# Performance work log

Measured on AMD Instinct MI355X. Metric: run time of the kernel, lower is better.

The kernel has to match this reference:

```python
import jax, jax.numpy as jnp
import numpy as np

B, S, H = 4, 2048, 1024
NH = 16
DH = H // NH  # 64


def setup_inputs() -> dict:
    key = jax.random.key(0)
    ks = jax.random.split(key, 11)
    s = 1.0 / np.sqrt(H)
    inp = {
        "key": jax.random.normal(ks[0], (B, S, H), jnp.float32),
        "value": jax.random.normal(ks[1], (B, S, H), jnp.float32),
        "query": jax.random.normal(ks[2], (B, S, H), jnp.float32),
        # linear_layers[0] -> applied to query, [1] -> key, [2] -> value
        "wq": jax.random.normal(ks[3], (H, H), jnp.float32) * s,
        "bq": jnp.zeros((H,), jnp.float32),
        "wk": jax.random.normal(ks[4], (H, H), jnp.float32) * s,
        "bk": jnp.zeros((H,), jnp.float32),
        "wv": jax.random.normal(ks[5], (H, H), jnp.float32) * s,
        "bv": jnp.zeros((H,), jnp.float32),
        "wo": jax.random.normal(ks[6], (H, H), jnp.float32) * s,
        "bo": jnp.zeros((H,), jnp.float32),
    }
    return inp


def reference(key, value, query, wq, bq, wk, bk, wv, bv, wo, bo):
    # QKV projections; split heads -> [B, NH, S, DH]
    def proj(x, w, b):
        y = jnp.einsum("bsh,hd->bsd", x, w) + b
        return y.reshape(B, S, NH, DH).transpose(0, 2, 1, 3)

    q = proj(query, wq, bq)
    k = proj(key, wk, bk)
    v = proj(value, wv, bv)

    scores = jnp.einsum("bnqd,bnkd->bnqk", q, k) / jnp.sqrt(jnp.float32(DH))
    probs = jax.nn.softmax(scores, axis=-1)  # dropout p=0 -> identity
    out = jnp.einsum("bnqk,bnkd->bnqd", probs, v)
    out = out.transpose(0, 2, 1, 3).reshape(B, S, H)
    return jnp.einsum("bsh,hd->bsd", out, wo) + bo
```

## Files before the change

### kernel.cpp

```cpp
#include <hip/hip_runtime.h>
#include <hip/hip_bf16.h>

constexpr int kB = 4, kS = 2048, kH = 1024, kNH = 16, kDH = 64;
constexpr int kM = kB * kS;

typedef short short8 __attribute__((ext_vector_type(8)));
typedef float f32x4 __attribute__((ext_vector_type(4)));

__device__ inline unsigned int pack2bf16(float lo, float hi) {
  __hip_bfloat162 h;
  h.x = __float2bfloat16(lo);
  h.y = __float2bfloat16(hi);
  unsigned int u;
  __builtin_memcpy(&u, &h, 4);
  return u;
}

__device__ inline void gload_lds16(const unsigned short* g, unsigned short* l) {
  auto* gp = (const __attribute__((address_space(1))) unsigned int*)(uintptr_t)g;
  auto* lp = (__attribute__((address_space(3))) unsigned int*)(unsigned int)(uintptr_t)l;
  __builtin_amdgcn_global_load_lds(gp, lp, 16, 0, 0);
}

__global__ __launch_bounds__(256) void f32_to_bf16_vec(
    const float* __restrict__ in, __hip_bfloat16* __restrict__ out) {
  const int i = blockIdx.x * 256 + threadIdx.x;
  const float4 v = ((const float4*)in)[i];
  union { __hip_bfloat16 h[4]; uint2 u; } p;
  p.h[0] = __float2bfloat16(v.x);
  p.h[1] = __float2bfloat16(v.y);
  p.h[2] = __float2bfloat16(v.z);
  p.h[3] = __float2bfloat16(v.w);
  ((uint2*)out)[i] = p.u;
}

__global__ __launch_bounds__(256) void transpose4_f32_to_bf16(
    const float* __restrict__ w0, const float* __restrict__ w1,
    const float* __restrict__ w2, const float* __restrict__ w3,
    __hip_bfloat16* __restrict__ o0, __hip_bfloat16* __restrict__ o1,
    __hip_bfloat16* __restrict__ o2, __hip_bfloat16* __restrict__ o3) {
  const int z = blockIdx.z;
  const float* in = z == 0 ? w0 : z == 1 ? w1 : z == 2 ? w2 : w3;
  __hip_bfloat16* out = z == 0 ? o0 : z == 1 ? o1 : z == 2 ? o2 : o3;
  constexpr int R = kH, C = kH;
  __shared__ float t[32][33];
  const int r0 = blockIdx.y * 32, c0 = blockIdx.x * 32;
  const int tx = threadIdx.x, ty = threadIdx.y;
#pragma unroll
  for (int i = 0; i < 32; i += 8)
    t[ty + i][tx] = in[(size_t)(r0 + ty + i) * C + c0 + tx];
  __syncthreads();
#pragma unroll
  for (int i = 0; i < 32; i += 8)
    out[(size_t)(c0 + ty + i) * R + r0 + tx] = __float2bfloat16(t[tx][ty + i]);
}

template <int MODE, typename OutT>
__global__ __launch_bounds__(256) void gemm_mfma(
    const unsigned short* __restrict__ A,
    const unsigned short* __restrict__ Bt,
    const float* __restrict__ bias, OutT* __restrict__ C,
    int M, int N, int K, float oscale) {
  __shared__ unsigned short sA[2][128 * 32];
  __shared__ unsigned short sB[2][128 * 32];
  const int tid = threadIdx.x;
  const int wave = tid >> 6, lane = tid & 63;
  const int n16 = lane & 15, quad = lane >> 4;
  const int m0 = blockIdx.y * 128, n0 = blockIdx.x * 128;
  const int rh = (wave >> 1) * 64, ch = (wave & 1) * 64;

  const int srow = 32 * wave + (lane >> 2);
  const int sk = (lane & 3) * 8;
  const unsigned short* gA = A + (size_t)(m0 + srow) * K + sk;
  const unsigned short* gB = Bt + (size_t)(n0 + srow) * K + sk;

  const f32x4 zero4 = {0.f, 0.f, 0.f, 0.f};
  f32x4 acc[4][4];
#pragma unroll
  for (int i = 0; i < 4; ++i)
#pragma unroll
    for (int j = 0; j < 4; ++j) acc[i][j] = zero4;

#pragma unroll
  for (int j = 0; j < 2; ++j) {
    gload_lds16(gA + (size_t)(16 * j) * K, &sA[0][(32 * wave + 16 * j) * 32]);
    gload_lds16(gB + (size_t)(16 * j) * K, &sB[0][(32 * wave + 16 * j) * 32]);
  }
  __syncthreads();

  int cur = 0;
  for (int k0 = 0; k0 < K; k0 += 32) {
    const int kn = (k0 + 32 < K) ? k0 + 32 : 0;
#pragma unroll
    for (int j = 0; j < 2; ++j) {
      gload_lds16(gA + (size_t)(16 * j) * K + kn,
                  &sA[cur ^ 1][(32 * wave + 16 * j) * 32]);
      gload_lds16(gB + (size_t)(16 * j) * K + kn,
                  &sB[cur ^ 1][(32 * wave + 16 * j) * 32]);
    }

    short8 af[4], bfr[4];
#pragma unroll
    for (int i = 0; i < 4; ++i)
      af[i] = *(const short8*)&sA[cur][(rh + i * 16 + n16) * 32 + quad * 8];
#pragma unroll
    for (int i = 0; i < 4; ++i)
      bfr[i] = *(const short8*)&sB[cur][(ch + i * 16 + n16) * 32 + quad * 8];
#pragma unroll
    for (int mi = 0; mi < 4; ++mi)
#pragma unroll
      for (int ni = 0; ni < 4; ++ni)
        acc[mi][ni] = __builtin_amdgcn_mfma_f32_16x16x32_bf16(
            af[mi], bfr[ni], acc[mi][ni], 0, 0, 0);

    __syncthreads();
    cur ^= 1;
  }

#pragma unroll
  for (int ni = 0; ni < 4; ++ni) {
    const int n = n0 + ch + ni * 16 + n16;
    const float bv = bias[n];
#pragma unroll
    for (int mi = 0; mi < 4; ++mi) {
      if constexpr (MODE == 2) {
        const int m = m0 + rh + mi * 16 + quad * 4;
        const int bb = m >> 11, ss = m & 2047;
        const int hh = n >> 6, dd = n & 63;
        const size_t idx = ((size_t)(bb * kNH + hh) * kDH + dd) * kS + ss;
        uint2 w;
        w.x = pack2bf16((acc[mi][ni][0] + bv) * oscale,
                        (acc[mi][ni][1] + bv) * oscale);
        w.y = pack2bf16((acc[mi][ni][2] + bv) * oscale,
                        (acc[mi][ni][3] + bv) * oscale);
        *(uint2*)&C[idx] = w;
      } else {
#pragma unroll
        for (int r = 0; r < 4; ++r) {
          const int m = m0 + rh + mi * 16 + quad * 4 + r;
          const float v = (acc[mi][ni][r] + bv) * oscale;
          size_t idx;
          if constexpr (MODE == 1) {
            const int bb = m >> 11, ss = m & 2047;
            const int hh = n >> 6, dd = n & 63;
            idx = ((size_t)(bb * kNH + hh) * kS + ss) * kDH + dd;
          } else {
            idx = (size_t)m * N + n;
          }
          C[idx] = (OutT)v;
        }
      }
    }
  }
}

__global__ __launch_bounds__(256) void attn_mfma(
    const unsigned short* __restrict__ Q, const unsigned short* __restrict__ K,
    const unsigned short* __restrict__ V, __hip_bfloat16* __restrict__ ctx) {
  __shared__ unsigned short sK[64][72];
  __shared__ unsigned short sVT[64][72];
  __shared__ unsigned short sP[4][16][72];

  const int tid = threadIdx.x;
  const int wave = tid >> 6, lane = tid & 63;
  const int n16 = lane & 15, quad = lane >> 4;
  const int bh = blockIdx.y;
  const int q0 = blockIdx.x * 64;
  const unsigned short* Qb = Q + (size_t)bh * (kS * kDH);
  const unsigned short* Kb = K + (size_t)bh * (kS * kDH);
  const unsigned short* Vb = V + (size_t)bh * (kS * kDH);

  short8 qf[2];
  {
    const size_t qoff = (size_t)(q0 + wave * 16 + n16) * kDH + quad * 8;
    qf[0] = *(const short8*)(Qb + qoff);
    qf[1] = *(const short8*)(Qb + qoff + 32);
  }

  float l_part = 0.f;
  f32x4 oacc[4];
  const f32x4 zero4 = {0.f, 0.f, 0.f, 0.f};
#pragma unroll
  for (int d = 0; d < 4; ++d) oacc[d] = zero4;

  const int srow = tid >> 2, scol = (tid & 3) * 16;

  uint4 ka, kb, va, vb;
  auto loadtile = [&](int kk) {
    ka = *(const uint4*)(Kb + (size_t)(kk + srow) * kDH + scol);
    kb = *(const uint4*)(Kb + (size_t)(kk + srow) * kDH + scol + 8);
    va = *(const uint4*)(Vb + (size_t)srow * kS + kk + scol);
    vb = *(const uint4*)(Vb + (size_t)srow * kS + kk + scol + 8);
  };
  auto writetile = [&]() {
    *(uint4*)&sK[srow][scol] = ka;
    *(uint4*)&sK[srow][scol + 8] = kb;
    *(uint4*)&sVT[srow][scol] = va;
    *(uint4*)&sVT[srow][scol + 8] = vb;
  };

  loadtile(0);
  writetile();
  __syncthreads();

  for (int k0 = 0; k0 < kS; k0 += 64) {
    const int kn = (k0 + 64 < kS) ? k0 + 64 : 0;
    loadtile(kn);

    f32x4 sacc[4] = {zero4, zero4, zero4, zero4};
    __builtin_amdgcn_s_setprio(1);
#pragma unroll
    for (int c = 0; c < 2; ++c) {
#pragma unroll
      for (int nb = 0; nb < 4; ++nb) {
        const short8 af = *(const short8*)&sK[nb * 16 + n16][c * 32 + quad * 8];
        sacc[nb] = __builtin_amdgcn_mfma_f32_16x16x32_bf16(af, qf[c], sacc[nb], 0, 0, 0);
      }
    }
    __builtin_amdgcn_s_setprio(0);

#pragma unroll
    for (int nb = 0; nb < 4; ++nb) {
      float p0 = __builtin_amdgcn_exp2f(sacc[nb][0]);
      float p1 = __builtin_amdgcn_exp2f(sacc[nb][1]);
      float p2 = __builtin_amdgcn_exp2f(sacc[nb][2]);
      float p3 = __builtin_amdgcn_exp2f(sacc[nb][3]);
      l_part += (p0 + p1) + (p2 + p3);
      uint2 w;
      w.x = pack2bf16(p0, p1);
      w.y = pack2bf16(p2, p3);
      *(uint2*)&sP[wave][n16][nb * 16 + quad * 4] = w;
    }
    asm volatile("s_waitcnt lgkmcnt(0)" ::: "memory");
    __builtin_amdgcn_sched_barrier(0);

    __builtin_amdgcn_s_setprio(1);
#pragma unroll
    for (int c = 0; c < 2; ++c) {
      const short8 pf = *(const short8*)&sP[wave][n16][c * 32 + quad * 8];
#pragma unroll
      for (int d = 0; d < 4; ++d) {
        const short8 vf = *(const short8*)&sVT[d * 16 + n16][c * 32 + quad * 8];
        oacc[d] = __builtin_amdgcn_mfma_f32_16x16x32_bf16(vf, pf, oacc[d], 0, 0, 0);
      }
    }
    __builtin_amdgcn_s_setprio(0);

    __syncthreads();
    writetile();
    __syncthreads();
  }

  float l = l_part;
  l += __shfl_xor(l, 16);
  l += __shfl_xor(l, 32);
  const float inv = 1.f / l;

  const int bb = bh >> 4, hh = bh & 15;
  const int qrow = q0 + wave * 16 + n16;
  __hip_bfloat16* dst = ctx + ((size_t)(bb * kS + qrow)) * kH + hh * kDH;
#pragma unroll
  for (int d = 0; d < 4; ++d) {
    uint2 w;
    w.x = pack2bf16(oacc[d][0] * inv, oacc[d][1] * inv);
    w.y = pack2bf16(oacc[d][2] * inv, oacc[d][3] * inv);
    *(uint2*)(dst + d * 16 + quad * 4) = w;
  }
}

extern "C" void kernel_launch(void* const* d_in, const int* in_sizes, int n_in,
                              void* d_out, int out_size, void* d_ws, size_t ws_size,
                              hipStream_t stream) {
  const float* key   = (const float*)d_in[0];
  const float* value = (const float*)d_in[1];
  const float* query = (const float*)d_in[2];
  const float* wq = (const float*)d_in[3];
  const float* bq = (const float*)d_in[4];
  const float* wk = (const float*)d_in[5];
  const float* bk = (const float*)d_in[6];
  const float* wv = (const float*)d_in[7];
  const float* bv = (const float*)d_in[8];
  const float* wo = (const float*)d_in[9];
  const float* bo = (const float*)d_in[10];
  float* out = (float*)d_out;

  const size_t SZ = (size_t)kB * kS * kH;
  unsigned short* p = (unsigned short*)d_ws;
  unsigned short* actb = p; p += SZ;
  unsigned short* Qh   = p; p += SZ;
  unsigned short* Kh   = p; p += SZ;
  unsigned short* Vh   = p; p += SZ;
  unsigned short* ctxh = p; p += SZ;
  unsigned short* wqt  = p; p += (size_t)kH * kH;
  unsigned short* wkt  = p; p += (size_t)kH * kH;
  unsigned short* wvt  = p; p += (size_t)kH * kH;
  unsigned short* wot  = p; p += (size_t)kH * kH;

  const dim3 tb(32, 8);
  const dim3 tg(kH / 32, kH / 32, 4);
  transpose4_f32_to_bf16<<<tg, tb, 0, stream>>>(
      wq, wk, wv, wo, (__hip_bfloat16*)wqt, (__hip_bfloat16*)wkt,
      (__hip_bfloat16*)wvt, (__hip_bfloat16*)wot);

  const int cvblocks = (int)(SZ / 4 / 256);
  dim3 gg(kH / 128, kM / 128);

  constexpr float kQScale = 0.125f * 1.4426950408889634f;
  f32_to_bf16_vec<<<cvblocks, 256, 0, stream>>>(query, (__hip_bfloat16*)actb);
  gemm_mfma<1, __hip_bfloat16><<<gg, 256, 0, stream>>>(
      actb, wqt, bq, (__hip_bfloat16*)Qh, kM, kH, kH, kQScale);
  f32_to_bf16_vec<<<cvblocks, 256, 0, stream>>>(key, (__hip_bfloat16*)actb);
  gemm_mfma<1, __hip_bfloat16><<<gg, 256, 0, stream>>>(
      actb, wkt, bk, (__hip_bfloat16*)Kh, kM, kH, kH, 1.0f);
  f32_to_bf16_vec<<<cvblocks, 256, 0, stream>>>(value, (__hip_bfloat16*)actb);
  gemm_mfma<2, __hip_bfloat16><<<gg, 256, 0, stream>>>(
      actb, wvt, bv, (__hip_bfloat16*)Vh, kM, kH, kH, 1.0f);

  dim3 ga(kS / 64, kB * kNH);
  attn_mfma<<<ga, 256, 0, stream>>>(Qh, Kh, Vh, (__hip_bfloat16*)ctxh);

  gemm_mfma<0, float><<<gg, 256, 0, stream>>>(ctxh, wot, bo, out, kM, kH, kH, 1.0f);
}
```

Baseline: 407.6 us.

## Batch QKV conversion and projections into single launches with XCD-aware block remapping

Merges the three fp32-to-bf16 activation conversions into one launch and the three Q/K/V projection GEMMs into one 3D-grid launch, reusing the ctx and output buffers as scratch for the converted key and value activations. Block IDs in the QKV GEMM, output GEMM and attention kernel are remapped so neighbouring tiles land on the same XCD, which should improve L2 reuse of shared weight and K/V tiles. This removes launch gaps and exposes more parallelism per launch. In exchange it adds occupancy hints and runtime branching on the projection index, and it depends on the scratch aliasing staying safe.

```diff
diff --git a/kernel.cpp b/kernel.cpp
--- a/kernel.cpp
+++ b/kernel.cpp
@@ -22,8 +22,13 @@
   __builtin_amdgcn_global_load_lds(gp, lp, 16, 0, 0);
 }
 
-__global__ __launch_bounds__(256) void f32_to_bf16_vec(
-    const float* __restrict__ in, __hip_bfloat16* __restrict__ out) {
+__global__ __launch_bounds__(256) void f32_to_bf16_vec3(
+    const float* __restrict__ i0, const float* __restrict__ i1,
+    const float* __restrict__ i2, __hip_bfloat16* __restrict__ o0,
+    __hip_bfloat16* __restrict__ o1, __hip_bfloat16* __restrict__ o2) {
+  const int z = blockIdx.y;
+  const float* in = z == 0 ? i0 : z == 1 ? i1 : i2;
+  __hip_bfloat16* out = z == 0 ? o0 : z == 1 ? o1 : o2;
   const int i = blockIdx.x * 256 + threadIdx.x;
   const float4 v = ((const float4*)in)[i];
   union { __hip_bfloat16 h[4]; uint2 u; } p;
@@ -55,24 +60,35 @@
     out[(size_t)(c0 + ty + i) * R + r0 + tx] = __float2bfloat16(t[tx][ty + i]);
 }
 
-template <int MODE, typename OutT>
-__global__ __launch_bounds__(256) void gemm_mfma(
-    const unsigned short* __restrict__ A,
-    const unsigned short* __restrict__ Bt,
-    const float* __restrict__ bias, OutT* __restrict__ C,
-    int M, int N, int K, float oscale) {
+__global__ __launch_bounds__(256, 4) void gemm_qkv(
+    const unsigned short* __restrict__ A0, const unsigned short* __restrict__ A1,
+    const unsigned short* __restrict__ A2, const unsigned short* __restrict__ W0,
+    const unsigned short* __restrict__ W1, const unsigned short* __restrict__ W2,
+    const float* __restrict__ b0, const float* __restrict__ b1,
+    const float* __restrict__ b2, unsigned short* __restrict__ O0,
+    unsigned short* __restrict__ O1, unsigned short* __restrict__ O2) {
+  constexpr int K = kH;
   __shared__ unsigned short sA[2][128 * 32];
   __shared__ unsigned short sB[2][128 * 32];
   const int tid = threadIdx.x;
   const int wave = tid >> 6, lane = tid & 63;
   const int n16 = lane & 15, quad = lane >> 4;
-  const int m0 = blockIdx.y * 128, n0 = blockIdx.x * 128;
+
+  const int hw = blockIdx.x + (blockIdx.y << 3) + ((int)blockIdx.z << 9);
+  const int wid = (hw & 7) * 192 + (hw >> 3);
+  const int z = wid >> 9;
+  const int rem = wid & 511;
+  const int n0 = (rem & 7) * 128, m0 = (rem >> 3) * 128;
+
+  const unsigned short* A = z == 0 ? A0 : z == 1 ? A1 : A2;
+  const unsigned short* W = z == 0 ? W0 : z == 1 ? W1 : W2;
+  const float* bias = z == 0 ? b0 : z == 1 ? b1 : b2;
+
   const int rh = (wave >> 1) * 64, ch = (wave & 1) * 64;
-
   const int srow = 32 * wave + (lane >> 2);
   const int sk = (lane & 3) * 8;
   const unsigned short* gA = A + (size_t)(m0 + srow) * K + sk;
-  const unsigned short* gB = Bt + (size_t)(n0 + srow) * K + sk;
+  const unsigned short* gB = W + (size_t)(n0 + srow) * K + sk;
 
   const f32x4 zero4 = {0.f, 0.f, 0.f, 0.f};
   f32x4 acc[4][4];
@@ -117,38 +133,107 @@
     cur ^= 1;
   }
 
+  __hip_bfloat16* Obf = (__hip_bfloat16*)(z == 0 ? O0 : z == 1 ? O1 : O2);
+  const float osc = z == 0 ? 0.18033688011112042f : 1.0f;
 #pragma unroll
   for (int ni = 0; ni < 4; ++ni) {
     const int n = n0 + ch + ni * 16 + n16;
     const float bv = bias[n];
+    const int hh = n >> 6, dd = n & 63;
 #pragma unroll
     for (int mi = 0; mi < 4; ++mi) {
-      if constexpr (MODE == 2) {
-        const int m = m0 + rh + mi * 16 + quad * 4;
-        const int bb = m >> 11, ss = m & 2047;
-        const int hh = n >> 6, dd = n & 63;
+      const int mbase = m0 + rh + mi * 16 + quad * 4;
+      const int bb = mbase >> 11, ss = mbase & 2047;
+      if (z == 2) {
         const size_t idx = ((size_t)(bb * kNH + hh) * kDH + dd) * kS + ss;
         uint2 w;
-        w.x = pack2bf16((acc[mi][ni][0] + bv) * oscale,
-                        (acc[mi][ni][1] + bv) * oscale);
-        w.y = pack2bf16((acc[mi][ni][2] + bv) * oscale,
-                        (acc[mi][ni][3] + bv) * oscale);
-        *(uint2*)&C[idx] = w;
+        w.x = pack2bf16(acc[mi][ni][0] + bv, acc[mi][ni][1] + bv);
+        w.y = pack2bf16(acc[mi][ni][2] + bv, acc[mi][ni][3] + bv);
+        *(uint2*)&Obf[idx] = w;
       } else {
-#pragma unroll
-        for (int r = 0; r < 4; ++r) {
-          const int m = m0 + rh + mi * 16 + quad * 4 + r;
-          const float v = (acc[mi][ni][r] + bv) * oscale;
-          size_t idx;
-          if constexpr (MODE == 1) {
-            const int bb = m >> 11, ss = m & 2047;
-            const int hh = n >> 6, dd = n & 63;
-            idx = ((size_t)(bb * kNH + hh) * kS + ss) * kDH + dd;
-          } else {
-            idx = (size_t)m * N + n;
-          }
-          C[idx] = (OutT)v;
-        }
+        const size_t base = ((size_t)(bb * kNH + hh) * kS + ss) * kDH + dd;
+#pragma unroll
+        for (int r = 0; r < 4; ++r)
+          Obf[base + (size_t)r * kDH] =
+              __float2bfloat16((acc[mi][ni][r] + bv) * osc);
+      }
+    }
+  }
+}
+
+__global__ __launch_bounds__(256) void gemm_out(
+    const unsigned short* __restrict__ A, const unsigned short* __restrict__ Bt,
+    const float* __restrict__ bias, float* __restrict__ C, int M, int N, int K) {
+  __shared__ unsigned short sA[2][128 * 32];
+  __shared__ unsigned short sB[2][128 * 32];
+  const int tid = threadIdx.x;
+  const int wave = tid >> 6, lane = tid & 63;
+  const int n16 = lane & 15, quad = lane >> 4;
+
+  const int hw = blockIdx.x + blockIdx.y * gridDim.x;
+  const int cpx = (gridDim.x * gridDim.y) >> 3;
+  const int wid = (hw & 7) * cpx + (hw >> 3);
+  const int n0 = (wid % gridDim.x) * 128, m0 = (wid / gridDim.x) * 128;
+
+  const int rh = (wave >> 1) * 64, ch = (wave & 1) * 64;
+  const int srow = 32 * wave + (lane >> 2);
+  const int sk = (lane & 3) * 8;
+  const unsigned short* gA = A + (size_t)(m0 + srow) * K + sk;
+  const unsigned short* gB = Bt + (size_t)(n0 + srow) * K + sk;
+
+  const f32x4 zero4 = {0.f, 0.f, 0.f, 0.f};
+  f32x4 acc[4][4];
+#pragma unroll
+  for (int i = 0; i < 4; ++i)
+#pragma unroll
+    for (int j = 0; j < 4; ++j) acc[i][j] = zero4;
+
+#pragma unroll
+  for (int j = 0; j < 2; ++j) {
+    gload_lds16(gA + (size_t)(16 * j) * K, &sA[0][(32 * wave + 16 * j) * 32]);
+    gload_lds16(gB + (size_t)(16 * j) * K, &sB[0][(32 * wave + 16 * j) * 32]);
+  }
+  __syncthreads();
+
+  int cur = 0;
+  for (int k0 = 0; k0 < K; k0 += 32) {
+    const int kn = (k0 + 32 < K) ? k0 + 32 : 0;
+#pragma unroll
+    for (int j = 0; j < 2; ++j) {
+      gload_lds16(gA + (size_t)(16 * j) * K + kn,
+                  &sA[cur ^ 1][(32 * wave + 16 * j) * 32]);
+      gload_lds16(gB + (size_t)(16 * j) * K + kn,
+                  &sB[cur ^ 1][(32 * wave + 16 * j) * 32]);
+    }
+
+    short8 af[4], bfr[4];
+#pragma unroll
+    for (int i = 0; i < 4; ++i)
+      af[i] = *(const short8*)&sA[cur][(rh + i * 16 + n16) * 32 + quad * 8];
+#pragma unroll
+    for (int i = 0; i < 4; ++i)
+      bfr[i] = *(const short8*)&sB[cur][(ch + i * 16 + n16) * 32 + quad * 8];
+#pragma unroll
+    for (int mi = 0; mi < 4; ++mi)
+#pragma unroll
+      for (int ni = 0; ni < 4; ++ni)
+        acc[mi][ni] = __builtin_amdgcn_mfma_f32_16x16x32_bf16(
+            af[mi], bfr[ni], acc[mi][ni], 0, 0, 0);
+
+    __syncthreads();
+    cur ^= 1;
+  }
+
+#pragma unroll
+  for (int ni = 0; ni < 4; ++ni) {
+    const int n = n0 + ch + ni * 16 + n16;
+    const float bv = bias[n];
+#pragma unroll
+    for (int mi = 0; mi < 4; ++mi) {
+#pragma unroll
+      for (int r = 0; r < 4; ++r) {
+        const int m = m0 + rh + mi * 16 + quad * 4 + r;
+        C[(size_t)m * N + n] = acc[mi][ni][r] + bv;
       }
     }
   }
@@ -164,8 +249,12 @@
   const int tid = threadIdx.x;
   const int wave = tid >> 6, lane = tid & 63;
   const int n16 = lane & 15, quad = lane >> 4;
-  const int bh = blockIdx.y;
-  const int q0 = blockIdx.x * 64;
+
+  const int hw = blockIdx.x + ((int)blockIdx.y << 5);
+  const int wid = (hw & 7) * 256 + (hw >> 3);
+  const int bh = wid >> 5;
+  const int q0 = (wid & 31) * 64;
+
   const unsigned short* Qb = Q + (size_t)bh * (kS * kDH);
   const unsigned short* Kb = K + (size_t)bh * (kS * kDH);
   const unsigned short* Vb = V + (size_t)bh * (kS * kDH);
@@ -295,6 +384,8 @@
   unsigned short* wkt  = p; p += (size_t)kH * kH;
   unsigned short* wvt  = p; p += (size_t)kH * kH;
   unsigned short* wot  = p; p += (size_t)kH * kH;
+  unsigned short* actk = ctxh;
+  unsigned short* actv = (unsigned short*)out;
 
   const dim3 tb(32, 8);
   const dim3 tg(kH / 32, kH / 32, 4);
@@ -303,21 +394,16 @@
       (__hip_bfloat16*)wvt, (__hip_bfloat16*)wot);
 
   const int cvblocks = (int)(SZ / 4 / 256);
-  dim3 gg(kH / 128, kM / 128);
-
-  constexpr float kQScale = 0.125f * 1.4426950408889634f;
-  f32_to_bf16_vec<<<cvblocks, 256, 0, stream>>>(query, (__hip_bfloat16*)actb);
-  gemm_mfma<1, __hip_bfloat16><<<gg, 256, 0, stream>>>(
-      actb, wqt, bq, (__hip_bfloat16*)Qh, kM, kH, kH, kQScale);
-  f32_to_bf16_vec<<<cvblocks, 256, 0, stream>>>(key, (__hip_bfloat16*)actb);
-  gemm_mfma<1, __hip_bfloat16><<<gg, 256, 0, stream>>>(
-      actb, wkt, bk, (__hip_bfloat16*)Kh, kM, kH, kH, 1.0f);
-  f32_to_bf16_vec<<<cvblocks, 256, 0, stream>>>(value, (__hip_bfloat16*)actb);
-  gemm_mfma<2, __hip_bfloat16><<<gg, 256, 0, stream>>>(
-      actb, wvt, bv, (__hip_bfloat16*)Vh, kM, kH, kH, 1.0f);
+  f32_to_bf16_vec3<<<dim3(cvblocks, 3), 256, 0, stream>>>(
+      query, key, value, (__hip_bfloat16*)actb, (__hip_bfloat16*)actk,
+      (__hip_bfloat16*)actv);
+
+  gemm_qkv<<<dim3(kH / 128, kM / 128, 3), 256, 0, stream>>>(
+      actb, actk, actv, wqt, wkt, wvt, bq, bk, bv, Qh, Kh, Vh);
 
   dim3 ga(kS / 64, kB * kNH);
   attn_mfma<<<ga, 256, 0, stream>>>(Qh, Kh, Vh, (__hip_bfloat16*)ctxh);
 
-  gemm_mfma<0, float><<<gg, 256, 0, stream>>>(ctxh, wot, bo, out, kM, kH, kH, 1.0f);
-}
+  dim3 gg(kH / 128, kM / 128);
+  gemm_out<<<gg, 256, 0, stream>>>(ctxh, wot, bo, out, kM, kH, kH);
+}
```

Result: faster. 382.4 us (-6.2%).
